# Kernel optimization log

Hardware: AMD Instinct MI355X
Metric: run time of the kernel (lower is better)

Reference implementation:

```python
import jax, jax.numpy as jnp
import numpy as np

N = 20000       # nodes
E = 320000      # edges
D_IN = 128
H = 512
OUT = 7
EPS = 1e-5


def setup_inputs() -> dict:
    key = jax.random.key(0)
    ks = jax.random.split(key, 16)
    def lin(k, fan_in, fan_out):
        bound = 1.0 / np.sqrt(fan_in)
        kw, kb = jax.random.split(k)
        W = jax.random.uniform(kw, (fan_in, fan_out), jnp.float32, -bound, bound)
        b = jax.random.uniform(kb, (fan_out,), jnp.float32, -bound, bound)
        return W, b
    x = jax.random.normal(ks[0], (N, D_IN), jnp.float32)
    edge_index = jax.random.randint(ks[1], (2, E), 0, N, dtype=jnp.int64)
    W1, b1 = lin(ks[2], D_IN, H)
    W2, b2 = lin(ks[3], H, H)
    W3, b3 = lin(ks[4], H, H)
    W4, b4 = lin(ks[5], H, H)
    ln_gamma = jnp.ones((H,), jnp.float32)
    ln_beta = jnp.zeros((H,), jnp.float32)
    W_out, b_out = lin(ks[6], H, OUT)
    return {"x": x, "edge_index": edge_index,
            "W1": W1, "b1": b1, "W2": W2, "b2": b2,
            "W3": W3, "b3": b3, "W4": W4, "b4": b4,
            "ln_gamma": ln_gamma, "ln_beta": ln_beta,
            "W_out": W_out, "b_out": b_out}


def _gcn_layer(x, W, b, src, dst, dinv):
    # transform, then symmetric-normalized gather/scatter-add (PyG GCNConv)
    h = x @ W                                    # [N, H]
    norm = dinv[src] * dinv[dst]                 # [E+N]
    msg = h[src] * norm[:, None]                 # gather + scale
    agg = jax.ops.segment_sum(msg, dst, num_segments=N)
    return agg + b


def reference(x, edge_index, W1, b1, W2, b2, W3, b3, W4, b4,
              ln_gamma, ln_beta, W_out, b_out):
    loops = jnp.arange(N, dtype=edge_index.dtype)
    src = jnp.concatenate([edge_index[0], loops])  # A + I self loops
    dst = jnp.concatenate([edge_index[1], loops])
    deg = jax.ops.segment_sum(jnp.ones_like(src, dtype=x.dtype), dst,
                              num_segments=N)
    dinv = jnp.where(deg > 0, jax.lax.rsqrt(deg), 0.0)

    def ln(h):
        mu = h.mean(-1, keepdims=True)
        var = h.var(-1, keepdims=True)
        return (h - mu) * jax.lax.rsqrt(var + EPS) * ln_gamma + ln_beta

    for W, b in ((W1, b1), (W2, b2), (W3, b3), (W4, b4)):
        x = jax.nn.relu(ln(_gcn_layer(x, W, b, src, dst, dinv)))
    g = x.mean(axis=0)           # mean pool over nodes -> [H]
    # dropout is identity in eval mode
    return g @ W_out + b_out     # [OUT]
```

## Files before the change

kernel.cpp:

```cpp
#include <hip/hip_runtime.h>

#define HID 512
#define OUTD 7
#define EPSV 1e-5f

typedef __attribute__((ext_vector_type(8))) short bf16x8;
typedef __attribute__((ext_vector_type(4))) float f32x4;
typedef __attribute__((ext_vector_type(2))) float f32x2;
typedef unsigned short ushort_t;
typedef unsigned int uint_t;
typedef unsigned char uchar_t;

__device__ __forceinline__ ushort_t f2bf(float f) {
    uint_t u = __float_as_uint(f);
    u = (u + 0x7fffu + ((u >> 16) & 1u)) >> 16;
    return (ushort_t)u;
}
__device__ __forceinline__ float bflo(uint_t u) { return __uint_as_float(u << 16); }
__device__ __forceinline__ float bfhi(uint_t u) { return __uint_as_float(u & 0xffff0000u); }

__device__ __forceinline__ void dec4(uint_t v, float* f) {
    f32x2 p0 = __builtin_amdgcn_cvt_pk_f32_fp8(v, false);
    f32x2 p1 = __builtin_amdgcn_cvt_pk_f32_fp8(v, true);
    f[0] = p0.x; f[1] = p0.y; f[2] = p1.x; f[3] = p1.y;
}
__device__ __forceinline__ uint_t enc4(float a, float b, float c, float d) {
    uint_t r = __builtin_amdgcn_cvt_pk_fp8_f32(a, b, 0, false);
    r = __builtin_amdgcn_cvt_pk_fp8_f32(c, d, r, true);
    return r;
}

__device__ __forceinline__ void gload_lds16(const ushort_t* g, ushort_t* l) {
    __builtin_amdgcn_global_load_lds(
        (const __attribute__((address_space(1))) uint_t*)g,
        (__attribute__((address_space(3))) uint_t*)l, 16, 0, 0);
}
__device__ __forceinline__ void gload_lds16_u8(const uchar_t* g, uchar_t* l) {
    __builtin_amdgcn_global_load_lds(
        (const __attribute__((address_space(1))) uint_t*)g,
        (__attribute__((address_space(3))) uint_t*)l, 16, 0, 0);
}


__global__ void zero_deg(int* __restrict__ deg, int N) {
    int i = blockIdx.x * blockDim.x + threadIdx.x;
    if (i < N) deg[i] = 0;
}

__global__ void setup2(const int* __restrict__ dst, int* __restrict__ deg, int E,
                       const float* __restrict__ W0, const float* __restrict__ W1,
                       const float* __restrict__ W2, const float* __restrict__ W3,
                       ushort_t* __restrict__ T0, ushort_t* __restrict__ T1,
                       ushort_t* __restrict__ T2, ushort_t* __restrict__ T3) {
    int i = blockIdx.x * blockDim.x + threadIdx.x;
    if (i < E) { atomicAdd(&deg[dst[i]], 1); return; }
    i -= E;
    const int S0 = 128 * HID, S1 = HID * HID;
    if (i < S0) { int k = i / HID, n = i % HID; T0[(size_t)n * 128 + k] = f2bf(W0[i]); return; }
    i -= S0;
    if (i < S1) { int k = i / HID, n = i % HID; T1[(size_t)n * HID + k] = f2bf(W1[i]); return; }
    i -= S1;
    if (i < S1) { int k = i / HID, n = i % HID; T2[(size_t)n * HID + k] = f2bf(W2[i]); return; }
    i -= S1;
    if (i < S1) { int k = i / HID, n = i % HID; T3[(size_t)n * HID + k] = f2bf(W3[i]); }
}


__global__ void scan1(const int* __restrict__ deg, int* __restrict__ off,
                      int* __restrict__ partial, float* __restrict__ dinv, int N) {
    __shared__ int s[256];
    const int t = threadIdx.x;
    const int i = blockIdx.x * 256 + t;
    int d = (i < N) ? deg[i] : 0;
    if (i < N) dinv[i] = rsqrtf((float)(d + 1));
    s[t] = d;
    __syncthreads();
#pragma unroll
    for (int ofs = 1; ofs < 256; ofs <<= 1) {
        int v = (t >= ofs) ? s[t - ofs] : 0;
        __syncthreads();
        s[t] += v;
        __syncthreads();
    }
    if (i < N) off[i] = s[t] - d;
    if (t == 255) partial[blockIdx.x] = s[255];
}

__global__ void scan23(int* __restrict__ off, const int* __restrict__ partial,
                       int* __restrict__ cursor, int N, int E, int nb) {
    __shared__ int s[256];
    __shared__ int ex[256];
    const int t = threadIdx.x;
    int d = (t < nb) ? partial[t] : 0;
    s[t] = d;
    __syncthreads();
#pragma unroll
    for (int ofs = 1; ofs < 256; ofs <<= 1) {
        int v = (t >= ofs) ? s[t - ofs] : 0;
        __syncthreads();
        s[t] += v;
        __syncthreads();
    }
    ex[t] = s[t] - d;
    __syncthreads();
    int i = blockIdx.x * 256 + t;
    if (i < N) {
        int v = off[i] + ex[i >> 8];
        off[i] = v;
        cursor[i] = v;
    } else if (i == N) {
        off[N] = E;
    }
}


__global__ void fill_cvt(const int* __restrict__ src, const int* __restrict__ dst,
                         int* __restrict__ cursor, int* __restrict__ srcs, int E,
                         const float* __restrict__ x, const float* __restrict__ dinv,
                         ushort_t* __restrict__ xb, int pairs, float* __restrict__ gsum) {
    int i = blockIdx.x * blockDim.x + threadIdx.x;
    if (i < E) { int p = atomicAdd(&cursor[dst[i]], 1); srcs[p] = src[i]; return; }
    i -= E;
    if (i < pairs) {
        float dr = dinv[i >> 6];
        float a = x[2 * i] * dr, b = x[2 * i + 1] * dr;
        uint_t d = __builtin_amdgcn_cvt_pk_fp8_f32(a, b, 0, false);
        xb[i] = (ushort_t)(d & 0xffffu);
        return;
    }
    i -= pairs;
    if (i < HID) gsum[i] = 0.0f;
}


__global__ __launch_bounds__(256) void csr_agg_512(
        const uchar_t* __restrict__ xs, const int* __restrict__ off,
        const int* __restrict__ srcs, const float* __restrict__ dinv,
        uchar_t* __restrict__ ax, int N) {
    int gtid = blockIdx.x * 256 + threadIdx.x;
    int r = gtid >> 6, lane = gtid & 63;
    if (r >= N) return;
    const uint2* xb = (const uint2*)xs;
    float a[8];
    {
        uint2 v = xb[(size_t)r * 64 + lane];
        dec4(v.x, a); dec4(v.y, a + 4);
    }
    int e = off[r];
    const int e1 = off[r + 1];
    for (; e + 8 <= e1; e += 8) {
        int si[8]; uint2 vi[8];
#pragma unroll
        for (int j = 0; j < 8; j++) si[j] = srcs[e + j];
#pragma unroll
        for (int j = 0; j < 8; j++) vi[j] = xb[(size_t)si[j] * 64 + lane];
#pragma unroll
        for (int j = 0; j < 8; j++) {
            float f[8]; dec4(vi[j].x, f); dec4(vi[j].y, f + 4);
#pragma unroll
            for (int q = 0; q < 8; q++) a[q] += f[q];
        }
    }
    for (; e < e1; e++) {
        uint2 v = xb[(size_t)srcs[e] * 64 + lane];
        float f[8]; dec4(v.x, f); dec4(v.y, f + 4);
#pragma unroll
        for (int q = 0; q < 8; q++) a[q] += f[q];
    }
    float dr = dinv[r];
    uint2 o;
    o.x = enc4(a[0] * dr, a[1] * dr, a[2] * dr, a[3] * dr);
    o.y = enc4(a[4] * dr, a[5] * dr, a[6] * dr, a[7] * dr);
    ((uint2*)ax)[(size_t)r * 64 + lane] = o;
}

__global__ __launch_bounds__(256) void csr_agg_128(
        const uchar_t* __restrict__ xs, const int* __restrict__ off,
        const int* __restrict__ srcs, const float* __restrict__ dinv,
        uchar_t* __restrict__ ax, int N) {
    int gtid = blockIdx.x * 256 + threadIdx.x;
    int r = gtid >> 6, lane = gtid & 63;
    if (r >= N) return;
    const ushort_t* xb = (const ushort_t*)xs;
    float a0, a1;
    {
        uint_t v = xb[(size_t)r * 64 + lane];
        f32x2 p = __builtin_amdgcn_cvt_pk_f32_fp8(v, false);
        a0 = p.x; a1 = p.y;
    }
    int e = off[r];
    const int e1 = off[r + 1];
    for (; e + 8 <= e1; e += 8) {
        int si[8]; uint_t vi[8];
#pragma unroll
        for (int j = 0; j < 8; j++) si[j] = srcs[e + j];
#pragma unroll
        for (int j = 0; j < 8; j++) vi[j] = xb[(size_t)si[j] * 64 + lane];
#pragma unroll
        for (int j = 0; j < 8; j++) {
            f32x2 p = __builtin_amdgcn_cvt_pk_f32_fp8(vi[j], false);
            a0 += p.x; a1 += p.y;
        }
    }
    for (; e < e1; e++) {
        uint_t v = xb[(size_t)srcs[e] * 64 + lane];
        f32x2 p = __builtin_amdgcn_cvt_pk_f32_fp8(v, false);
        a0 += p.x; a1 += p.y;
    }
    float dr = dinv[r];
    uint_t d = __builtin_amdgcn_cvt_pk_fp8_f32(a0 * dr, a1 * dr, 0, false);
    ((ushort_t*)ax)[(size_t)r * 64 + lane] = (ushort_t)(d & 0xffffu);
}


__global__ __launch_bounds__(256) void gemm_mfma(
        const uchar_t* __restrict__ A, const ushort_t* __restrict__ Wt,
        const float* __restrict__ bias, ushort_t* __restrict__ C, int M, int K) {
    __shared__ __align__(16) uchar_t  As[4 * 128 * 16];
    __shared__ __align__(16) ushort_t Bs[8 * 128 * 8];
    const int t = threadIdx.x;
    const int wave = t >> 6, lane = t & 63;
    const int m0 = blockIdx.y * 128, n0 = blockIdx.x * 128;
    const int wm = (wave & 1) * 64, wn = (wave >> 1) * 64;
    const int quad = lane >> 4, l16 = lane & 15;

    f32x4 acc[4][4];
#pragma unroll
    for (int i = 0; i < 4; i++)
#pragma unroll
        for (int j = 0; j < 4; j++) acc[i][j] = (f32x4){0.f, 0.f, 0.f, 0.f};

    for (int k0 = 0; k0 < K; k0 += 64) {
#pragma unroll
        for (int h = 0; h < 2; h++) {
            int gm = m0 + 64 * h + lane;
            if (gm >= M) gm = M - 1;
            gload_lds16_u8(A + (size_t)gm * K + k0 + wave * 16,
                           &As[(wave * 128 + 64 * h) * 16]);
        }
#pragma unroll
        for (int h = 0; h < 4; h++) {
            int cb = wave * 2 + (h >> 1);
            int row = (h & 1) * 64 + lane;
            gload_lds16(Wt + (size_t)(n0 + row) * K + k0 + cb * 8,
                        &Bs[(cb * 128 + (h & 1) * 64) * 8]);
        }
        __syncthreads();
#pragma unroll
        for (int kk = 0; kk < 2; kk++) {
            bf16x8 af[4], bfr[4];
#pragma unroll
            for (int jn = 0; jn < 4; jn++)
                bfr[jn] = *(const bf16x8*)&Bs[((kk * 4 + quad) * 128 + wn + jn * 16 + l16) * 8];
#pragma unroll
            for (int i = 0; i < 4; i++) {
                uint2 v8 = *(const uint2*)&As[((kk * 2 + (quad >> 1)) * 128 + wm + i * 16 + l16) * 16
                                              + (quad & 1) * 8];
                f32x2 p0 = __builtin_amdgcn_cvt_pk_f32_fp8(v8.x, false);
                f32x2 p1 = __builtin_amdgcn_cvt_pk_f32_fp8(v8.x, true);
                f32x2 p2 = __builtin_amdgcn_cvt_pk_f32_fp8(v8.y, false);
                f32x2 p3 = __builtin_amdgcn_cvt_pk_f32_fp8(v8.y, true);
                union { uint_t u[4]; bf16x8 v; } pk;
                pk.u[0] = (__float_as_uint(p0.y) & 0xffff0000u) | (__float_as_uint(p0.x) >> 16);
                pk.u[1] = (__float_as_uint(p1.y) & 0xffff0000u) | (__float_as_uint(p1.x) >> 16);
                pk.u[2] = (__float_as_uint(p2.y) & 0xffff0000u) | (__float_as_uint(p2.x) >> 16);
                pk.u[3] = (__float_as_uint(p3.y) & 0xffff0000u) | (__float_as_uint(p3.x) >> 16);
                af[i] = pk.v;
            }
#pragma unroll
            for (int i = 0; i < 4; i++)
#pragma unroll
                for (int jn = 0; jn < 4; jn++)
                    acc[i][jn] = __builtin_amdgcn_mfma_f32_16x16x32_bf16(
                                     af[i], bfr[jn], acc[i][jn], 0, 0, 0);
        }
        __syncthreads();
    }
#pragma unroll
    for (int i = 0; i < 4; i++) {
#pragma unroll
        for (int jn = 0; jn < 4; jn++) {
            int gn = n0 + wn + jn * 16 + l16;
            float bv = bias[gn];
#pragma unroll
            for (int rg = 0; rg < 4; rg++) {
                int gm = m0 + wm + i * 16 + quad * 4 + rg;
                if (gm < M) C[(size_t)gm * HID + gn] = f2bf(acc[i][jn][rg] + bv);
            }
        }
    }
}


template<int MODE>
__global__ void ln_relu(const ushort_t* __restrict__ h, const float* __restrict__ gamma,
                        const float* __restrict__ beta, const float* __restrict__ dinv,
                        void* __restrict__ optr, int N) {
    int gtid = blockIdx.x * blockDim.x + threadIdx.x;
    int r = gtid >> 6, lane = gtid & 63;
    if (r >= N) return;
    uint4 v = ((const uint4*)(h + (size_t)r * HID))[lane];
    float f[8] = {bflo(v.x), bfhi(v.x), bflo(v.y), bfhi(v.y),
                  bflo(v.z), bfhi(v.z), bflo(v.w), bfhi(v.w)};
    float s = 0.f, q = 0.f;
#pragma unroll
    for (int j = 0; j < 8; j++) { s += f[j]; q += f[j] * f[j]; }
#pragma unroll
    for (int ofs = 32; ofs > 0; ofs >>= 1) {
        s += __shfl_xor(s, ofs);
        q += __shfl_xor(q, ofs);
    }
    float mu  = s * (1.0f / HID);
    float var = q * (1.0f / HID) - mu * mu;
    float rs  = rsqrtf(var + EPSV);
    float dr  = (MODE == 1) ? dinv[r] : 1.0f;
    const float4* gp = (const float4*)gamma;
    const float4* bp = (const float4*)beta;
    float4 g0 = gp[2 * lane], g1 = gp[2 * lane + 1];
    float4 b0 = bp[2 * lane], b1 = bp[2 * lane + 1];
    float gg[8] = {g0.x, g0.y, g0.z, g0.w, g1.x, g1.y, g1.z, g1.w};
    float bb[8] = {b0.x, b0.y, b0.z, b0.w, b1.x, b1.y, b1.z, b1.w};
    float o[8];
#pragma unroll
    for (int j = 0; j < 8; j++)
        o[j] = fmaxf((f[j] - mu) * rs * gg[j] + bb[j], 0.f) * dr;
    if (MODE == 0) {
        uint4 ov;
        ov.x = (uint_t)f2bf(o[0]) | ((uint_t)f2bf(o[1]) << 16);
        ov.y = (uint_t)f2bf(o[2]) | ((uint_t)f2bf(o[3]) << 16);
        ov.z = (uint_t)f2bf(o[4]) | ((uint_t)f2bf(o[5]) << 16);
        ov.w = (uint_t)f2bf(o[6]) | ((uint_t)f2bf(o[7]) << 16);
        ((uint4*)optr)[(size_t)r * 64 + lane] = ov;
    } else {
        uint2 ov;
        ov.x = enc4(o[0], o[1], o[2], o[3]);
        ov.y = enc4(o[4], o[5], o[6], o[7]);
        ((uint2*)optr)[(size_t)r * 64 + lane] = ov;
    }
}


__global__ void colsum(const ushort_t* __restrict__ h, float* __restrict__ gsum, int N) {
    int t = threadIdx.x;
    float a0 = 0.f, a1 = 0.f;
    for (int r = blockIdx.x; r < N; r += gridDim.x) {
        uint_t u = ((const uint_t*)(h + (size_t)r * HID))[t];
        a0 += bflo(u);
        a1 += bfhi(u);
    }
    atomicAdd(&gsum[2 * t], a0);
    atomicAdd(&gsum[2 * t + 1], a1);
}

__global__ void out_kernel(const float* __restrict__ gsum, const float* __restrict__ Wout,
                           const float* __restrict__ bout, float* __restrict__ out, int N) {
    __shared__ float red[256];
    int t = threadIdx.x;
    float g0 = gsum[2 * t], g1 = gsum[2 * t + 1];
    float invn = 1.0f / (float)N;
    for (int o = 0; o < OUTD; o++) {
        float p = g0 * Wout[(2 * t) * OUTD + o] + g1 * Wout[(2 * t + 1) * OUTD + o];
        red[t] = p;
        __syncthreads();
        for (int sft = 128; sft > 0; sft >>= 1) {
            if (t < sft) red[t] += red[t + sft];
            __syncthreads();
        }
        if (t == 0) out[o] = red[0] * invn + bout[o];
        __syncthreads();
    }
}


extern "C" void kernel_launch(void* const* d_in, const int* in_sizes, int n_in,
                              void* d_out, int out_size, void* d_ws, size_t ws_size,
                              hipStream_t stream) {
    const float* x  = (const float*)d_in[0];
    const int*   ei = (const int*)d_in[1];
    const int N = in_sizes[0] / 128;
    const int E = in_sizes[1] / 2;
    const int* src = ei;
    const int* dst = ei + E;
    const float* Ws[4] = {(const float*)d_in[2], (const float*)d_in[4],
                          (const float*)d_in[6], (const float*)d_in[8]};
    const float* bs[4] = {(const float*)d_in[3], (const float*)d_in[5],
                          (const float*)d_in[7], (const float*)d_in[9]};
    const float* gamma = (const float*)d_in[10];
    const float* beta  = (const float*)d_in[11];
    const float* Wout  = (const float*)d_in[12];
    const float* bout  = (const float*)d_in[13];
    float* out = (float*)d_out;

    char* p = (char*)d_ws;
    uchar_t*  axb = (uchar_t*)p;   p += (size_t)N * HID;
    ushort_t* hb  = (ushort_t*)p;  p += sizeof(ushort_t) * (size_t)N * HID;
    uchar_t*  ho8 = (uchar_t*)p;   p += (size_t)N * HID;
    uchar_t*  xb8 = ho8;
    ushort_t* Wt[4];
    Wt[0] = (ushort_t*)p;          p += sizeof(ushort_t) * 128 * HID;
    Wt[1] = (ushort_t*)p;          p += sizeof(ushort_t) * HID * HID;
    Wt[2] = (ushort_t*)p;          p += sizeof(ushort_t) * HID * HID;
    Wt[3] = (ushort_t*)p;          p += sizeof(ushort_t) * HID * HID;
    float* dinv = (float*)p;       p += sizeof(float) * N;
    float* gsum = (float*)p;       p += sizeof(float) * HID;
    int* deg    = (int*)p;         p += sizeof(int) * N;
    int* off    = (int*)p;         p += sizeof(int) * (N + 4);
    int* cursor = (int*)p;         p += sizeof(int) * N;
    int* partial= (int*)p;         p += sizeof(int) * 256;
    int* srcs   = (int*)p;

    const int nb = (N + 255) / 256;

    zero_deg<<<(N + 255) / 256, 256, 0, stream>>>(deg, N);
    {
        int tot = E + 128 * HID + 3 * HID * HID;
        setup2<<<(tot + 255) / 256, 256, 0, stream>>>(dst, deg, E, Ws[0], Ws[1], Ws[2], Ws[3],
                                                      Wt[0], Wt[1], Wt[2], Wt[3]);
    }
    scan1<<<nb, 256, 0, stream>>>(deg, off, partial, dinv, N);
    scan23<<<(N + 256) / 256, 256, 0, stream>>>(off, partial, cursor, N, E, nb);
    {
        int pairs = N * 64;
        int tot = E + pairs + HID;
        fill_cvt<<<(tot + 255) / 256, 256, 0, stream>>>(src, dst, cursor, srcs, E,
                                                        x, dinv, (ushort_t*)xb8, pairs, gsum);
    }

    for (int l = 0; l < 4; l++) {
        const int K = (l == 0) ? 128 : HID;
        if (l == 0)
            csr_agg_128<<<(N * 64 + 255) / 256, 256, 0, stream>>>(xb8, off, srcs, dinv, axb, N);
        else
            csr_agg_512<<<(N * 64 + 255) / 256, 256, 0, stream>>>(ho8, off, srcs, dinv, axb, N);
        dim3 gg(HID / 128, (N + 127) / 128);
        gemm_mfma<<<gg, 256, 0, stream>>>(axb, Wt[l], bs[l], hb, N, K);
        if (l < 3)
            ln_relu<1><<<(N * 64 + 255) / 256, 256, 0, stream>>>(hb, gamma, beta, dinv, ho8, N);
        else
            ln_relu<0><<<(N * 64 + 255) / 256, 256, 0, stream>>>(hb, gamma, beta, dinv, hb, N);
    }
    colsum<<<512, 256, 0, stream>>>(hb, gsum, N);
    out_kernel<<<1, 256, 0, stream>>>(gsum, Wout, bout, out, N);
}
```

Baseline: 395.3 us.

## Widen CSR gather loads to 16 bytes and fuse final LayerNorm with mean pooling

```diff
diff --git a/kernel.cpp b/kernel.cpp
--- a/kernel.cpp
+++ b/kernel.cpp
@@ -140,38 +140,54 @@
     int gtid = blockIdx.x * 256 + threadIdx.x;
     int r = gtid >> 6, lane = gtid & 63;
     if (r >= N) return;
-    const uint2* xb = (const uint2*)xs;
-    float a[8];
-    {
-        uint2 v = xb[(size_t)r * 64 + lane];
-        dec4(v.x, a); dec4(v.y, a + 4);
+    const int half = lane >> 5, l32 = lane & 31;
+    const uint4* xb = (const uint4*)xs;
+    float a[16];
+    if (half == 0) {
+        uint4 v = xb[(size_t)r * 32 + l32];
+        dec4(v.x, a); dec4(v.y, a + 4); dec4(v.z, a + 8); dec4(v.w, a + 12);
+    } else {
+#pragma unroll
+        for (int q = 0; q < 16; q++) a[q] = 0.f;
     }
     int e = off[r];
     const int e1 = off[r + 1];
     for (; e + 8 <= e1; e += 8) {
-        int si[8]; uint2 vi[8];
-#pragma unroll
-        for (int j = 0; j < 8; j++) si[j] = srcs[e + j];
-#pragma unroll
-        for (int j = 0; j < 8; j++) vi[j] = xb[(size_t)si[j] * 64 + lane];
-#pragma unroll
-        for (int j = 0; j < 8; j++) {
-            float f[8]; dec4(vi[j].x, f); dec4(vi[j].y, f + 4);
-#pragma unroll
-            for (int q = 0; q < 8; q++) a[q] += f[q];
-        }
-    }
-    for (; e < e1; e++) {
-        uint2 v = xb[(size_t)srcs[e] * 64 + lane];
-        float f[8]; dec4(v.x, f); dec4(v.y, f + 4);
-#pragma unroll
-        for (int q = 0; q < 8; q++) a[q] += f[q];
-    }
-    float dr = dinv[r];
-    uint2 o;
-    o.x = enc4(a[0] * dr, a[1] * dr, a[2] * dr, a[3] * dr);
-    o.y = enc4(a[4] * dr, a[5] * dr, a[6] * dr, a[7] * dr);
-    ((uint2*)ax)[(size_t)r * 64 + lane] = o;
+        int si[4]; uint4 vi[4];
+#pragma unroll
+        for (int j = 0; j < 4; j++) si[j] = srcs[e + 2 * j + half];
+#pragma unroll
+        for (int j = 0; j < 4; j++) vi[j] = xb[(size_t)si[j] * 32 + l32];
+#pragma unroll
+        for (int j = 0; j < 4; j++) {
+            float f[16];
+            dec4(vi[j].x, f); dec4(vi[j].y, f + 4); dec4(vi[j].z, f + 8); dec4(vi[j].w, f + 12);
+#pragma unroll
+            for (int q = 0; q < 16; q++) a[q] += f[q];
+        }
+    }
+    for (; e < e1; e += 2) {
+        int idx = e + half;
+        bool valid = idx < e1;
+        int s = srcs[valid ? idx : e];
+        uint4 v = xb[(size_t)s * 32 + l32];
+        if (!valid) { v.x = 0; v.y = 0; v.z = 0; v.w = 0; }
+        float f[16];
+        dec4(v.x, f); dec4(v.y, f + 4); dec4(v.z, f + 8); dec4(v.w, f + 12);
+#pragma unroll
+        for (int q = 0; q < 16; q++) a[q] += f[q];
+    }
+#pragma unroll
+    for (int q = 0; q < 16; q++) a[q] += __shfl_xor(a[q], 32);
+    if (half == 0) {
+        float dr = dinv[r];
+        uint4 o;
+        o.x = enc4(a[0] * dr,  a[1] * dr,  a[2] * dr,  a[3] * dr);
+        o.y = enc4(a[4] * dr,  a[5] * dr,  a[6] * dr,  a[7] * dr);
+        o.z = enc4(a[8] * dr,  a[9] * dr,  a[10] * dr, a[11] * dr);
+        o.w = enc4(a[12] * dr, a[13] * dr, a[14] * dr, a[15] * dr);
+        ((uint4*)ax)[(size_t)r * 32 + l32] = o;
+    }
 }
 
 __global__ __launch_bounds__(256) void csr_agg_128(
@@ -181,35 +197,43 @@
     int gtid = blockIdx.x * 256 + threadIdx.x;
     int r = gtid >> 6, lane = gtid & 63;
     if (r >= N) return;
-    const ushort_t* xb = (const ushort_t*)xs;
-    float a0, a1;
-    {
-        uint_t v = xb[(size_t)r * 64 + lane];
-        f32x2 p = __builtin_amdgcn_cvt_pk_f32_fp8(v, false);
-        a0 = p.x; a1 = p.y;
-    }
-    int e = off[r];
+    const int sub = lane >> 3, l8 = lane & 7;
+    const uint4* xb = (const uint4*)xs;
+    float a[16];
+    if (sub == 0) {
+        uint4 v = xb[(size_t)r * 8 + l8];
+        dec4(v.x, a); dec4(v.y, a + 4); dec4(v.z, a + 8); dec4(v.w, a + 12);
+    } else {
+#pragma unroll
+        for (int q = 0; q < 16; q++) a[q] = 0.f;
+    }
     const int e1 = off[r + 1];
-    for (; e + 8 <= e1; e += 8) {
-        int si[8]; uint_t vi[8];
-#pragma unroll
-        for (int j = 0; j < 8; j++) si[j] = srcs[e + j];
-#pragma unroll
-        for (int j = 0; j < 8; j++) vi[j] = xb[(size_t)si[j] * 64 + lane];
-#pragma unroll
-        for (int j = 0; j < 8; j++) {
-            f32x2 p = __builtin_amdgcn_cvt_pk_f32_fp8(vi[j], false);
-            a0 += p.x; a1 += p.y;
-        }
-    }
-    for (; e < e1; e++) {
-        uint_t v = xb[(size_t)srcs[e] * 64 + lane];
-        f32x2 p = __builtin_amdgcn_cvt_pk_f32_fp8(v, false);
-        a0 += p.x; a1 += p.y;
-    }
-    float dr = dinv[r];
-    uint_t d = __builtin_amdgcn_cvt_pk_fp8_f32(a0 * dr, a1 * dr, 0, false);
-    ((ushort_t*)ax)[(size_t)r * 64 + lane] = (ushort_t)(d & 0xffffu);
+    for (int e = off[r]; e < e1; e += 8) {
+        int idx = e + sub;
+        bool valid = idx < e1;
+        int s = srcs[valid ? idx : e];
+        uint4 v = xb[(size_t)s * 8 + l8];
+        if (!valid) { v.x = 0; v.y = 0; v.z = 0; v.w = 0; }
+        float f[16];
+        dec4(v.x, f); dec4(v.y, f + 4); dec4(v.z, f + 8); dec4(v.w, f + 12);
+#pragma unroll
+        for (int q = 0; q < 16; q++) a[q] += f[q];
+    }
+#pragma unroll
+    for (int q = 0; q < 16; q++) a[q] += __shfl_xor(a[q], 8);
+#pragma unroll
+    for (int q = 0; q < 16; q++) a[q] += __shfl_xor(a[q], 16);
+#pragma unroll
+    for (int q = 0; q < 16; q++) a[q] += __shfl_xor(a[q], 32);
+    if (sub == 0) {
+        float dr = dinv[r];
+        uint4 o;
+        o.x = enc4(a[0] * dr,  a[1] * dr,  a[2] * dr,  a[3] * dr);
+        o.y = enc4(a[4] * dr,  a[5] * dr,  a[6] * dr,  a[7] * dr);
+        o.z = enc4(a[8] * dr,  a[9] * dr,  a[10] * dr, a[11] * dr);
+        o.w = enc4(a[12] * dr, a[13] * dr, a[14] * dr, a[15] * dr);
+        ((uint4*)ax)[(size_t)r * 8 + l8] = o;
+    }
 }
 
 
@@ -292,7 +316,6 @@
 }
 
 
-template<int MODE>
 __global__ void ln_relu(const ushort_t* __restrict__ h, const float* __restrict__ gamma,
                         const float* __restrict__ beta, const float* __restrict__ dinv,
                         void* __restrict__ optr, int N) {
@@ -313,7 +336,7 @@
     float mu  = s * (1.0f / HID);
     float var = q * (1.0f / HID) - mu * mu;
     float rs  = rsqrtf(var + EPSV);
-    float dr  = (MODE == 1) ? dinv[r] : 1.0f;
+    float dr  = dinv[r];
     const float4* gp = (const float4*)gamma;
     const float4* bp = (const float4*)beta;
     float4 g0 = gp[2 * lane], g1 = gp[2 * lane + 1];
@@ -324,33 +347,58 @@
 #pragma unroll
     for (int j = 0; j < 8; j++)
         o[j] = fmaxf((f[j] - mu) * rs * gg[j] + bb[j], 0.f) * dr;
-    if (MODE == 0) {
-        uint4 ov;
-        ov.x = (uint_t)f2bf(o[0]) | ((uint_t)f2bf(o[1]) << 16);
-        ov.y = (uint_t)f2bf(o[2]) | ((uint_t)f2bf(o[3]) << 16);
-        ov.z = (uint_t)f2bf(o[4]) | ((uint_t)f2bf(o[5]) << 16);
-        ov.w = (uint_t)f2bf(o[6]) | ((uint_t)f2bf(o[7]) << 16);
-        ((uint4*)optr)[(size_t)r * 64 + lane] = ov;
-    } else {
-        uint2 ov;
-        ov.x = enc4(o[0], o[1], o[2], o[3]);
-        ov.y = enc4(o[4], o[5], o[6], o[7]);
-        ((uint2*)optr)[(size_t)r * 64 + lane] = ov;
-    }
-}
-
-
-__global__ void colsum(const ushort_t* __restrict__ h, float* __restrict__ gsum, int N) {
-    int t = threadIdx.x;
-    float a0 = 0.f, a1 = 0.f;
-    for (int r = blockIdx.x; r < N; r += gridDim.x) {
-        uint_t u = ((const uint_t*)(h + (size_t)r * HID))[t];
-        a0 += bflo(u);
-        a1 += bfhi(u);
-    }
-    atomicAdd(&gsum[2 * t], a0);
-    atomicAdd(&gsum[2 * t + 1], a1);
-}
+    uint2 ov;
+    ov.x = enc4(o[0], o[1], o[2], o[3]);
+    ov.y = enc4(o[4], o[5], o[6], o[7]);
+    ((uint2*)optr)[(size_t)r * 64 + lane] = ov;
+}
+
+
+__global__ __launch_bounds__(256) void ln_pool(
+        const ushort_t* __restrict__ h, const float* __restrict__ gamma,
+        const float* __restrict__ beta, float* __restrict__ gsum, int N) {
+    __shared__ float sred[4][64][8];
+    const int t = threadIdx.x;
+    const int sub = t >> 6, lane = t & 63;
+    const float4* gp = (const float4*)gamma;
+    const float4* bp = (const float4*)beta;
+    float4 g0 = gp[2 * lane], g1 = gp[2 * lane + 1];
+    float4 b0 = bp[2 * lane], b1 = bp[2 * lane + 1];
+    float gg[8] = {g0.x, g0.y, g0.z, g0.w, g1.x, g1.y, g1.z, g1.w};
+    float bb[8] = {b0.x, b0.y, b0.z, b0.w, b1.x, b1.y, b1.z, b1.w};
+    float colacc[8] = {0.f, 0.f, 0.f, 0.f, 0.f, 0.f, 0.f, 0.f};
+    const int step = gridDim.x * 4;
+    for (int r = blockIdx.x * 4 + sub; r < N; r += step) {
+        uint4 v = ((const uint4*)(h + (size_t)r * HID))[lane];
+        float f[8] = {bflo(v.x), bfhi(v.x), bflo(v.y), bfhi(v.y),
+                      bflo(v.z), bfhi(v.z), bflo(v.w), bfhi(v.w)};
+        float s = 0.f, q = 0.f;
+#pragma unroll
+        for (int j = 0; j < 8; j++) { s += f[j]; q += f[j] * f[j]; }
+#pragma unroll
+        for (int ofs = 32; ofs > 0; ofs >>= 1) {
+            s += __shfl_xor(s, ofs);
+            q += __shfl_xor(q, ofs);
+        }
+        float mu  = s * (1.0f / HID);
+        float var = q * (1.0f / HID) - mu * mu;
+        float rs  = rsqrtf(var + EPSV);
+#pragma unroll
+        for (int j = 0; j < 8; j++)
+            colacc[j] += fmaxf((f[j] - mu) * rs * gg[j] + bb[j], 0.f);
+    }
+#pragma unroll
+    for (int j = 0; j < 8; j++) sred[sub][lane][j] = colacc[j];
+    __syncthreads();
+    if (sub == 0) {
+#pragma unroll
+        for (int j = 0; j < 8; j++) {
+            float v = sred[0][lane][j] + sred[1][lane][j] + sred[2][lane][j] + sred[3][lane][j];
+            atomicAdd(&gsum[lane * 8 + j], v);
+        }
+    }
+}
+
 
 __global__ void out_kernel(const float* __restrict__ gsum, const float* __restrict__ Wout,
                            const float* __restrict__ bout, float* __restrict__ out, int N) {
@@ -435,10 +483,9 @@
         dim3 gg(HID / 128, (N + 127) / 128);
         gemm_mfma<<<gg, 256, 0, stream>>>(axb, Wt[l], bs[l], hb, N, K);
         if (l < 3)
-            ln_relu<1><<<(N * 64 + 255) / 256, 256, 0, stream>>>(hb, gamma, beta, dinv, ho8, N);
+            ln_relu<<<(N * 64 + 255) / 256, 256, 0, stream>>>(hb, gamma, beta, dinv, ho8, N);
         else
-            ln_relu<0><<<(N * 64 + 255) / 256, 256, 0, stream>>>(hb, gamma, beta, dinv, hb, N);
-    }
-    colsum<<<512, 256, 0, stream>>>(hb, gsum, N);
+            ln_pool<<<512, 256, 0, stream>>>(hb, gamma, beta, gsum, N);
+    }
     out_kernel<<<1, 256, 0, stream>>>(gsum, Wout, bout, out, N);
 }
```

Result: slower. 468.0 us (+18.4%).
